# Kernel optimization log

Hardware: AMD Instinct MI355X
Metric: run time of the kernel (lower is better)

Reference implementation:

```python
import jax, jax.numpy as jnp
import numpy as np

N, E, D = 50000, 600000, 128
LN_EPS = 1e-5


def setup_inputs() -> dict:
    key = jax.random.key(0)
    ks = jax.random.split(key, 7)
    s = 1.0 / np.sqrt(D)
    x = jax.random.normal(ks[0], (N, D), dtype=jnp.float32)
    edge_index = jax.random.randint(ks[1], (2, E), 0, N, dtype=jnp.int32)
    Wq = jax.random.normal(ks[2], (D, D), dtype=jnp.float32) * s
    Wk = jax.random.normal(ks[3], (D, D), dtype=jnp.float32) * s
    Wv = jax.random.normal(ks[4], (D, D), dtype=jnp.float32) * s
    Wo = jax.random.normal(ks[5], (D, D), dtype=jnp.float32) * s
    bo = jnp.zeros((D,), dtype=jnp.float32)
    gamma = jnp.ones((D,), dtype=jnp.float32)
    beta = jnp.zeros((D,), dtype=jnp.float32)
    return {"x": x, "edge_index": edge_index, "Wq": Wq, "Wk": Wk,
            "Wv": Wv, "Wo": Wo, "bo": bo, "gamma": gamma, "beta": beta}


def reference(x, edge_index, Wq, Wk, Wv, Wo, bo, gamma, beta):
    src, dst = edge_index[0], edge_index[1]
    # gather endpoint features, project (torch Linear: y = x @ W.T)
    q = x[dst] @ Wq.T                      # [E, D]
    k = x[src] @ Wk.T                      # [E, D]
    v = x[src] @ Wv.T                      # [E, D]
    logits = jnp.sum(q * k, axis=-1, keepdims=True) / np.sqrt(D)  # [E, 1]
    msg = jax.nn.sigmoid(logits) * v       # [E, D]
    agg = jax.ops.segment_sum(msg, dst, num_segments=N)  # scatter-add -> [N, D]
    out = agg @ Wo.T + bo
    h = x + out
    # LayerNorm over last dim
    mu = jnp.mean(h, axis=-1, keepdims=True)
    var = jnp.mean(jnp.square(h - mu), axis=-1, keepdims=True)
    return (h - mu) * jax.lax.rsqrt(var + LN_EPS) * gamma + beta
```

## Files before the change

### kernel.cpp

```cpp
#include <hip/hip_runtime.h>
#include <math.h>


#define BM 64
#define NB 8

typedef __attribute__((ext_vector_type(8))) short bfrag;
typedef __attribute__((ext_vector_type(4))) float f32x4;

__device__ __forceinline__ short f2bf(float f) {
    union { float f; unsigned u; } v; v.f = f;
    unsigned r = v.u + 0x7FFFu + ((v.u >> 16) & 1u);
    return (short)(r >> 16);
}
__device__ __forceinline__ float bf2f(short h) {
    union { unsigned u; float f; } v;
    v.u = ((unsigned)(unsigned short)h) << 16;
    return v.f;
}
__device__ __forceinline__ float2 bfpair(unsigned w) {
    union { unsigned u; float f; } lo, hi;
    lo.u = w << 16;
    hi.u = w & 0xffff0000u;
    return make_float2(lo.f, hi.f);
}

__global__ __launch_bounds__(256) void zero_prep(
    const float* __restrict__ Wq, const float* __restrict__ Wk,
    const float* __restrict__ Wv, const float* __restrict__ Wo,
    short* __restrict__ whi, short* __restrict__ wlo,
    int* __restrict__ hist, int N)
{
    int g = blockIdx.x * 256 + threadIdx.x;
    if (g < N) hist[g] = 0;
    if (g < 65536) {
        const float* Ws[4] = {Wq, Wk, Wv, Wo};
        float f = Ws[g >> 14][g & 16383];
        short h = f2bf(f);
        short l = f2bf(f - bf2f(h));
        whi[g] = h; wlo[g] = l;
    }
}

__global__ __launch_bounds__(256) void qkv_mfma(
    const float* __restrict__ x,
    const short* __restrict__ whi, const short* __restrict__ wlo,
    float* __restrict__ Q, unsigned short* __restrict__ KV16, int N)
{
    __shared__ short xs_hi[64][136];
    __shared__ short xs_lo[64][136];

    const int tid = threadIdx.x;
    const int row0 = blockIdx.x * BM;

    #pragma unroll
    for (int i = 0; i < 8; ++i) {
        int idx = tid + 256 * i;
        int r = idx >> 5;
        int c4 = idx & 31;
        int gr = row0 + r;
        float4 val = make_float4(0.f, 0.f, 0.f, 0.f);
        if (gr < N) val = ((const float4*)(x + (size_t)gr * 128))[c4];
        short4 h, l;
        h.x = f2bf(val.x); l.x = f2bf(val.x - bf2f(h.x));
        h.y = f2bf(val.y); l.y = f2bf(val.y - bf2f(h.y));
        h.z = f2bf(val.z); l.z = f2bf(val.z - bf2f(h.z));
        h.w = f2bf(val.w); l.w = f2bf(val.w - bf2f(h.w));
        *((short4*)&xs_hi[r][c4 * 4]) = h;
        *((short4*)&xs_lo[r][c4 * 4]) = l;
    }
    __syncthreads();

    const int wid  = tid >> 6;
    const int lane = tid & 63;
    const int n16  = lane & 15;
    const int quad = lane >> 4;

    #pragma unroll 1
    for (int mat = 0; mat < 3; ++mat) {
        const short* __restrict__ WH = whi + mat * 16384;
        const short* __restrict__ WL = wlo + mat * 16384;
        const f32x4 zero = {0.f, 0.f, 0.f, 0.f};
        f32x4 acc[4][2];
        #pragma unroll
        for (int t = 0; t < 4; ++t) { acc[t][0] = zero; acc[t][1] = zero; }

        #pragma unroll
        for (int kc = 0; kc < 4; ++kc) {
            int k0 = kc * 32 + quad * 8;
            bfrag ah[4], al[4], bh[2], bl[2];
            #pragma unroll
            for (int t = 0; t < 4; ++t) {
                ah[t] = *((const bfrag*)&xs_hi[t * 16 + n16][k0]);
                al[t] = *((const bfrag*)&xs_lo[t * 16 + n16][k0]);
            }
            #pragma unroll
            for (int c = 0; c < 2; ++c) {
                int wr = (wid * 2 + c) * 16 + n16;
                bh[c] = *((const bfrag*)(WH + wr * 128 + k0));
                bl[c] = *((const bfrag*)(WL + wr * 128 + k0));
            }
            #pragma unroll
            for (int t = 0; t < 4; ++t)
                #pragma unroll
                for (int c = 0; c < 2; ++c) {
                    acc[t][c] = __builtin_amdgcn_mfma_f32_16x16x32_bf16(ah[t], bh[c], acc[t][c], 0, 0, 0);
                    acc[t][c] = __builtin_amdgcn_mfma_f32_16x16x32_bf16(al[t], bh[c], acc[t][c], 0, 0, 0);
                    acc[t][c] = __builtin_amdgcn_mfma_f32_16x16x32_bf16(ah[t], bl[c], acc[t][c], 0, 0, 0);
                }
        }
        #pragma unroll
        for (int t = 0; t < 4; ++t)
            #pragma unroll
            for (int r = 0; r < 4; ++r) {
                int grow = row0 + t * 16 + quad * 4 + r;
                if (grow < N) {
                    int c0 = (wid * 2 + 0) * 16 + n16;
                    int c1 = (wid * 2 + 1) * 16 + n16;
                    if (mat == 0) {
                        Q[(size_t)grow * 128 + c0] = acc[t][0][r];
                        Q[(size_t)grow * 128 + c1] = acc[t][1][r];
                    } else {
                        size_t base = (size_t)grow * 256 + (mat - 1);
                        KV16[base + 2 * c0] = (unsigned short)f2bf(acc[t][0][r]);
                        KV16[base + 2 * c1] = (unsigned short)f2bf(acc[t][1][r]);
                    }
                }
            }
    }
}

__global__ __launch_bounds__(256) void hist_kernel(
    const int* __restrict__ ei, int* __restrict__ hist, int E)
{
    int e = blockIdx.x * blockDim.x + threadIdx.x;
    if (e < E) atomicAdd(&hist[ei[E + e]], 1);
}

#define SCAN_TPB 256
#define SCAN_EPT 4

__global__ __launch_bounds__(SCAN_TPB) void scan_partial(
    const int* __restrict__ hist, int* __restrict__ offs,
    int* __restrict__ blockSums, int N)
{
    __shared__ int sdata[SCAN_TPB];
    int b = blockIdx.x;
    int t = threadIdx.x;
    int base = b * SCAN_TPB * SCAN_EPT + t * SCAN_EPT;
    int v[SCAN_EPT];
    int tot = 0;
    #pragma unroll
    for (int j = 0; j < SCAN_EPT; ++j) {
        int idx = base + j;
        v[j] = (idx < N) ? hist[idx] : 0;
        tot += v[j];
    }
    sdata[t] = tot;
    __syncthreads();
    for (int off = 1; off < SCAN_TPB; off <<= 1) {
        int xv = (t >= off) ? sdata[t - off] : 0;
        __syncthreads();
        sdata[t] += xv;
        __syncthreads();
    }
    int run = sdata[t] - tot;
    #pragma unroll
    for (int j = 0; j < SCAN_EPT; ++j) {
        int idx = base + j;
        if (idx < N) offs[idx] = run;
        run += v[j];
    }
    if (t == SCAN_TPB - 1) blockSums[b] = sdata[t];
}

__global__ __launch_bounds__(256) void scan_blocksums(int* __restrict__ blockSums, int nb)
{
    __shared__ int sdata[256];
    int t = threadIdx.x;
    int orig = (t < nb) ? blockSums[t] : 0;
    sdata[t] = orig;
    __syncthreads();
    for (int off = 1; off < 256; off <<= 1) {
        int xv = (t >= off) ? sdata[t - off] : 0;
        __syncthreads();
        sdata[t] += xv;
        __syncthreads();
    }
    if (t < nb) blockSums[t] = sdata[t] - orig;
}

__global__ __launch_bounds__(256) void scan_add(
    int* __restrict__ offs, int* __restrict__ starts,
    const int* __restrict__ blockSums, int N)
{
    int idx = blockIdx.x * blockDim.x + threadIdx.x;
    if (idx < N) {
        int vv = offs[idx] + blockSums[idx >> 10];
        offs[idx] = vv;
        starts[idx] = vv;
    }
}

__global__ __launch_bounds__(256) void scatter_kernel(
    const int* __restrict__ ei, int* __restrict__ offs,
    int* __restrict__ ssrc, int E)
{
    int e = blockIdx.x * blockDim.x + threadIdx.x;
    if (e < E) {
        int d = ei[E + e];
        int pos = atomicAdd(&offs[d], 1);
        ssrc[pos] = ei[e];
    }
}

__global__ __launch_bounds__(256) void node_agg(
    const int* __restrict__ ssrc,
    const int* __restrict__ starts,
    const int* __restrict__ endoffs,
    const float* __restrict__ Q, const unsigned short* __restrict__ KV16,
    float* __restrict__ agg, int N)
{
    int node = blockIdx.x * 4 + (threadIdx.x >> 6);
    int lane = threadIdx.x & 63;
    if (node >= N) return;
    int start = starts[node];
    int end = endoffs[node];
    float2 q = *((const float2*)(Q + (size_t)node * 128 + lane * 2));
    float a0 = 0.f, a1 = 0.f;

    for (int i = start; i < end; i += NB) {
        int s[NB];
        #pragma unroll
        for (int j = 0; j < NB; ++j) {
            int idx = i + j;
            idx = (idx < end) ? idx : (end - 1);
            s[j] = ssrc[idx];
        }
        uint2 w[NB];
        #pragma unroll
        for (int j = 0; j < NB; ++j)
            w[j] = *((const uint2*)(KV16 + (size_t)s[j] * 256 + lane * 4));
        float p[NB];
        #pragma unroll
        for (int j = 0; j < NB; ++j) {
            float2 kv0 = bfpair(w[j].x);
            float2 kv1 = bfpair(w[j].y);
            p[j] = q.x * kv0.x + q.y * kv1.x;
        }
        #pragma unroll
        for (int j = 0; j < NB; ++j)
            p[j] += __int_as_float(__builtin_amdgcn_ds_swizzle(__float_as_int(p[j]), 0x041F));
        #pragma unroll
        for (int j = 0; j < NB; ++j)
            p[j] += __int_as_float(__builtin_amdgcn_ds_swizzle(__float_as_int(p[j]), 0x081F));
        #pragma unroll
        for (int j = 0; j < NB; ++j)
            p[j] += __int_as_float(__builtin_amdgcn_ds_swizzle(__float_as_int(p[j]), 0x101F));
        #pragma unroll
        for (int j = 0; j < NB; ++j)
            p[j] += __int_as_float(__builtin_amdgcn_ds_swizzle(__float_as_int(p[j]), 0x201F));
        #pragma unroll
        for (int j = 0; j < NB; ++j)
            p[j] += __int_as_float(__builtin_amdgcn_ds_swizzle(__float_as_int(p[j]), 0x401F));
        #pragma unroll
        for (int j = 0; j < NB; ++j)
            p[j] += __shfl_xor(p[j], 32);

        #pragma unroll
        for (int j = 0; j < NB; ++j) {
            float c = 1.f / (1.f + __expf(-p[j] * 0.0883883476483184f));
            if (i + j >= end) c = 0.f;
            float2 kv0 = bfpair(w[j].x);
            float2 kv1 = bfpair(w[j].y);
            a0 += c * kv0.y; a1 += c * kv1.y;
        }
    }
    *((float2*)(agg + (size_t)node * 128 + lane * 2)) = make_float2(a0, a1);
}

__global__ __launch_bounds__(256) void out_ln_mfma(
    const float* __restrict__ agg,
    const short* __restrict__ whi, const short* __restrict__ wlo,
    const float* __restrict__ bo, const float* __restrict__ x,
    const float* __restrict__ gamma, const float* __restrict__ beta,
    float* __restrict__ out, int N)
{
    __shared__ __align__(16) char smem[64 * 136 * 2 * 2];
    short (*xs_hi)[136] = (short(*)[136])smem;
    short (*xs_lo)[136] = (short(*)[136])(smem + 64 * 136 * 2);
    float (*hs)[132]    = (float(*)[132])smem;

    const int tid = threadIdx.x;
    const int row0 = blockIdx.x * BM;

    #pragma unroll
    for (int i = 0; i < 8; ++i) {
        int idx = tid + 256 * i;
        int r = idx >> 5;
        int c4 = idx & 31;
        int gr = row0 + r;
        float4 val = make_float4(0.f, 0.f, 0.f, 0.f);
        if (gr < N) val = ((const float4*)(agg + (size_t)gr * 128))[c4];
        short4 h, l;
        h.x = f2bf(val.x); l.x = f2bf(val.x - bf2f(h.x));
        h.y = f2bf(val.y); l.y = f2bf(val.y - bf2f(h.y));
        h.z = f2bf(val.z); l.z = f2bf(val.z - bf2f(h.z));
        h.w = f2bf(val.w); l.w = f2bf(val.w - bf2f(h.w));
        *((short4*)&xs_hi[r][c4 * 4]) = h;
        *((short4*)&xs_lo[r][c4 * 4]) = l;
    }
    __syncthreads();

    const int wid  = tid >> 6;
    const int lane = tid & 63;
    const int n16  = lane & 15;
    const int quad = lane >> 4;
    const short* __restrict__ WH = whi + 3 * 16384;
    const short* __restrict__ WL = wlo + 3 * 16384;

    const f32x4 zero = {0.f, 0.f, 0.f, 0.f};
    f32x4 acc[4][2];
    #pragma unroll
    for (int t = 0; t < 4; ++t) { acc[t][0] = zero; acc[t][1] = zero; }

    #pragma unroll
    for (int kc = 0; kc < 4; ++kc) {
        int k0 = kc * 32 + quad * 8;
        bfrag ah[4], al[4], bh[2], bl[2];
        #pragma unroll
        for (int t = 0; t < 4; ++t) {
            ah[t] = *((const bfrag*)&xs_hi[t * 16 + n16][k0]);
            al[t] = *((const bfrag*)&xs_lo[t * 16 + n16][k0]);
        }
        #pragma unroll
        for (int c = 0; c < 2; ++c) {
            int wr = (wid * 2 + c) * 16 + n16;
            bh[c] = *((const bfrag*)(WH + wr * 128 + k0));
            bl[c] = *((const bfrag*)(WL + wr * 128 + k0));
        }
        #pragma unroll
        for (int t = 0; t < 4; ++t)
            #pragma unroll
            for (int c = 0; c < 2; ++c) {
                acc[t][c] = __builtin_amdgcn_mfma_f32_16x16x32_bf16(ah[t], bh[c], acc[t][c], 0, 0, 0);
                acc[t][c] = __builtin_amdgcn_mfma_f32_16x16x32_bf16(al[t], bh[c], acc[t][c], 0, 0, 0);
                acc[t][c] = __builtin_amdgcn_mfma_f32_16x16x32_bf16(ah[t], bl[c], acc[t][c], 0, 0, 0);
            }
    }
    __syncthreads();

    #pragma unroll
    for (int t = 0; t < 4; ++t)
        #pragma unroll
        for (int r = 0; r < 4; ++r) {
            hs[t * 16 + quad * 4 + r][(wid * 2 + 0) * 16 + n16] = acc[t][0][r];
            hs[t * 16 + quad * 4 + r][(wid * 2 + 1) * 16 + n16] = acc[t][1][r];
        }
    __syncthreads();

    {
        int r = tid >> 2;
        int qd = tid & 3;
        int gr = row0 + r;
        float sum = 0.f, sq = 0.f;
        #pragma unroll
        for (int c = 0; c < 32; c += 4) {
            float4 g4 = *((float4*)&hs[r][qd * 32 + c]);
            float4 b4 = *((const float4*)(bo + qd * 32 + c));
            float4 x4 = make_float4(0.f, 0.f, 0.f, 0.f);
            if (gr < N) x4 = *((const float4*)(x + (size_t)gr * 128 + qd * 32 + c));
            float4 h = make_float4(g4.x + b4.x + x4.x, g4.y + b4.y + x4.y,
                                   g4.z + b4.z + x4.z, g4.w + b4.w + x4.w);
            *((float4*)&hs[r][qd * 32 + c]) = h;
            sum += h.x + h.y + h.z + h.w;
            sq += h.x * h.x + h.y * h.y + h.z * h.z + h.w * h.w;
        }
        sum += __shfl_xor(sum, 1); sum += __shfl_xor(sum, 2);
        sq  += __shfl_xor(sq, 1);  sq  += __shfl_xor(sq, 2);
        float mu = sum * (1.f / 128.f);
        float var = sq * (1.f / 128.f) - mu * mu;
        float rs = rsqrtf(var + 1e-5f);
        if (gr < N) {
            #pragma unroll
            for (int c = 0; c < 32; c += 4) {
                float4 h = *((float4*)&hs[r][qd * 32 + c]);
                float4 g = *((const float4*)(gamma + qd * 32 + c));
                float4 b = *((const float4*)(beta + qd * 32 + c));
                float4 o = make_float4((h.x - mu) * rs * g.x + b.x,
                                       (h.y - mu) * rs * g.y + b.y,
                                       (h.z - mu) * rs * g.z + b.z,
                                       (h.w - mu) * rs * g.w + b.w);
                *((float4*)(out + (size_t)gr * 128 + qd * 32 + c)) = o;
            }
        }
    }
}

extern "C" void kernel_launch(void* const* d_in, const int* in_sizes, int n_in,
                              void* d_out, int out_size, void* d_ws, size_t ws_size,
                              hipStream_t stream) {
    const float* x     = (const float*)d_in[0];
    const int*   ei    = (const int*)d_in[1];
    const float* Wq    = (const float*)d_in[2];
    const float* Wk    = (const float*)d_in[3];
    const float* Wv    = (const float*)d_in[4];
    const float* Wo    = (const float*)d_in[5];
    const float* bo    = (const float*)d_in[6];
    const float* gamma = (const float*)d_in[7];
    const float* beta  = (const float*)d_in[8];
    const int N = in_sizes[0] / 128;
    const int E = in_sizes[1] / 2;
    const size_t ND = (size_t)N * 128;

    float* ws  = (float*)d_ws;
    float* Q   = ws;
    unsigned short* KV16 = (unsigned short*)(Q + ND);
    float* agg = (float*)(KV16 + 2 * ND);
    int* hist      = (int*)(agg + ND);
    int* offs      = hist + N;
    int* starts    = offs + N;
    int* blockSums = starts + N;
    int* ssrc      = blockSums + 256;
    short* whi     = (short*)(ssrc + E);
    short* wlo     = whi + 4 * 16384;

    const int gzp = ((N > 65536 ? N : 65536) + 255) / 256;
    zero_prep<<<gzp, 256, 0, stream>>>(Wq, Wk, Wv, Wo, whi, wlo, hist, N);

    hist_kernel<<<(E + 255) / 256, 256, 0, stream>>>(ei, hist, E);
    const int nScanBlocks = (N + SCAN_TPB * SCAN_EPT - 1) / (SCAN_TPB * SCAN_EPT);
    scan_partial<<<nScanBlocks, SCAN_TPB, 0, stream>>>(hist, offs, blockSums, N);
    scan_blocksums<<<1, 256, 0, stream>>>(blockSums, nScanBlocks);
    scan_add<<<(N + 255) / 256, 256, 0, stream>>>(offs, starts, blockSums, N);
    scatter_kernel<<<(E + 255) / 256, 256, 0, stream>>>(ei, offs, ssrc, E);

    const int gq = (N + BM - 1) / BM;
    qkv_mfma<<<gq, 256, 0, stream>>>(x, whi, wlo, Q, KV16, N);

    node_agg<<<(N + 3) / 4, 256, 0, stream>>>(ssrc, starts, offs, Q, KV16, agg, N);

    out_ln_mfma<<<gq, 256, 0, stream>>>(agg, whi, wlo, bo, x, gamma, beta,
                                        (float*)d_out, N);
}
```

Measured before the change: 281.5 us.

## Split wavefront into 4 edge groups of 16 lanes in node aggregation

The node aggregation kernel now has each wavefront process 4 edges at a time, twice per iteration, with 16 lanes per edge. Each lane loads 32 bytes of interleaved K/V and reduces over 16 lanes instead of 64, so there are fewer swizzle steps per edge. Partial accumulators from the four edge groups are combined once at the end. The Q projection now stores Q pre-multiplied by the negated 1/sqrt(D) factor, and the sigmoid uses a fast reciprocal. This cuts cross-lane reduction work and raises memory parallelism per edge, at the cost of more registers and an extra reduction at the end.

Result: no change. 280.8 us (-0.2%).

```diff
diff --git a/kernel.cpp b/kernel.cpp
--- a/kernel.cpp
+++ b/kernel.cpp
@@ -3,7 +3,7 @@
 
 
 #define BM 64
-#define NB 8
+#define QSCALE -0.08838834764831845f
 
 typedef __attribute__((ext_vector_type(8))) short bfrag;
 typedef __attribute__((ext_vector_type(4))) float f32x4;
@@ -18,12 +18,14 @@
     v.u = ((unsigned)(unsigned short)h) << 16;
     return v.f;
 }
-__device__ __forceinline__ float2 bfpair(unsigned w) {
-    union { unsigned u; float f; } lo, hi;
-    lo.u = w << 16;
-    hi.u = w & 0xffff0000u;
-    return make_float2(lo.f, hi.f);
-}
+__device__ __forceinline__ float klo(unsigned w) {
+    union { unsigned u; float f; } v; v.u = w << 16; return v.f;
+}
+__device__ __forceinline__ float vhi(unsigned w) {
+    union { unsigned u; float f; } v; v.u = w & 0xffff0000u; return v.f;
+}
+
+#define SWZ(x, pat) __int_as_float(__builtin_amdgcn_ds_swizzle(__float_as_int(x), pat))
 
 __global__ __launch_bounds__(256) void zero_prep(
     const float* __restrict__ Wq, const float* __restrict__ Wk,
@@ -118,8 +120,8 @@
                     int c0 = (wid * 2 + 0) * 16 + n16;
                     int c1 = (wid * 2 + 1) * 16 + n16;
                     if (mat == 0) {
-                        Q[(size_t)grow * 128 + c0] = acc[t][0][r];
-                        Q[(size_t)grow * 128 + c1] = acc[t][1][r];
+                        Q[(size_t)grow * 128 + c0] = acc[t][0][r] * QSCALE;
+                        Q[(size_t)grow * 128 + c1] = acc[t][1][r] * QSCALE;
                     } else {
                         size_t base = (size_t)grow * 256 + (mat - 1);
                         KV16[base + 2 * c0] = (unsigned short)f2bf(acc[t][0][r]);
@@ -222,61 +224,88 @@
     float* __restrict__ agg, int N)
 {
     int node = blockIdx.x * 4 + (threadIdx.x >> 6);
+    if (node >= N) return;
     int lane = threadIdx.x & 63;
-    if (node >= N) return;
+    int eg   = lane >> 4;
+    int sl   = lane & 15;
     int start = starts[node];
-    int end = endoffs[node];
-    float2 q = *((const float2*)(Q + (size_t)node * 128 + lane * 2));
-    float a0 = 0.f, a1 = 0.f;
-
-    for (int i = start; i < end; i += NB) {
-        int s[NB];
-        #pragma unroll
-        for (int j = 0; j < NB; ++j) {
-            int idx = i + j;
-            idx = (idx < end) ? idx : (end - 1);
-            s[j] = ssrc[idx];
-        }
-        uint2 w[NB];
-        #pragma unroll
-        for (int j = 0; j < NB; ++j)
-            w[j] = *((const uint2*)(KV16 + (size_t)s[j] * 256 + lane * 4));
-        float p[NB];
-        #pragma unroll
-        for (int j = 0; j < NB; ++j) {
-            float2 kv0 = bfpair(w[j].x);
-            float2 kv1 = bfpair(w[j].y);
-            p[j] = q.x * kv0.x + q.y * kv1.x;
-        }
-        #pragma unroll
-        for (int j = 0; j < NB; ++j)
-            p[j] += __int_as_float(__builtin_amdgcn_ds_swizzle(__float_as_int(p[j]), 0x041F));
-        #pragma unroll
-        for (int j = 0; j < NB; ++j)
-            p[j] += __int_as_float(__builtin_amdgcn_ds_swizzle(__float_as_int(p[j]), 0x081F));
-        #pragma unroll
-        for (int j = 0; j < NB; ++j)
-            p[j] += __int_as_float(__builtin_amdgcn_ds_swizzle(__float_as_int(p[j]), 0x101F));
-        #pragma unroll
-        for (int j = 0; j < NB; ++j)
-            p[j] += __int_as_float(__builtin_amdgcn_ds_swizzle(__float_as_int(p[j]), 0x201F));
-        #pragma unroll
-        for (int j = 0; j < NB; ++j)
-            p[j] += __int_as_float(__builtin_amdgcn_ds_swizzle(__float_as_int(p[j]), 0x401F));
-        #pragma unroll
-        for (int j = 0; j < NB; ++j)
-            p[j] += __shfl_xor(p[j], 32);
-
-        #pragma unroll
-        for (int j = 0; j < NB; ++j) {
-            float c = 1.f / (1.f + __expf(-p[j] * 0.0883883476483184f));
-            if (i + j >= end) c = 0.f;
-            float2 kv0 = bfpair(w[j].x);
-            float2 kv1 = bfpair(w[j].y);
-            a0 += c * kv0.y; a1 += c * kv1.y;
-        }
-    }
-    *((float2*)(agg + (size_t)node * 128 + lane * 2)) = make_float2(a0, a1);
+    int end   = endoffs[node];
+
+    const float4 q0 = *((const float4*)(Q + (size_t)node * 128 + sl * 8));
+    const float4 q1 = *((const float4*)(Q + (size_t)node * 128 + sl * 8 + 4));
+
+    float a0 = 0.f, a1 = 0.f, a2 = 0.f, a3 = 0.f;
+    float a4 = 0.f, a5 = 0.f, a6 = 0.f, a7 = 0.f;
+
+    const unsigned short* kvbase = KV16 + sl * 16;
+
+    for (int i = start; i < end; i += 8) {
+        int i0 = i + eg;
+        int i1 = i + 4 + eg;
+        int ok0 = (i0 < end);
+        int ok1 = (i1 < end);
+        i0 = ok0 ? i0 : (end - 1);
+        i1 = ok1 ? i1 : (end - 1);
+        int s0 = ssrc[i0];
+        int s1 = ssrc[i1];
+        const unsigned short* kp0 = kvbase + ((size_t)s0 << 8);
+        const unsigned short* kp1 = kvbase + ((size_t)s1 << 8);
+        uint4 wa0 = *((const uint4*)kp0);
+        uint4 wa1 = *((const uint4*)(kp0 + 8));
+        uint4 wb0 = *((const uint4*)kp1);
+        uint4 wb1 = *((const uint4*)(kp1 + 8));
+
+        float p0, p1;
+        p0 = q0.x * klo(wa0.x);
+        p0 = fmaf(q0.y, klo(wa0.y), p0);
+        p0 = fmaf(q0.z, klo(wa0.z), p0);
+        p0 = fmaf(q0.w, klo(wa0.w), p0);
+        p0 = fmaf(q1.x, klo(wa1.x), p0);
+        p0 = fmaf(q1.y, klo(wa1.y), p0);
+        p0 = fmaf(q1.z, klo(wa1.z), p0);
+        p0 = fmaf(q1.w, klo(wa1.w), p0);
+        p1 = q0.x * klo(wb0.x);
+        p1 = fmaf(q0.y, klo(wb0.y), p1);
+        p1 = fmaf(q0.z, klo(wb0.z), p1);
+        p1 = fmaf(q0.w, klo(wb0.w), p1);
+        p1 = fmaf(q1.x, klo(wb1.x), p1);
+        p1 = fmaf(q1.y, klo(wb1.y), p1);
+        p1 = fmaf(q1.z, klo(wb1.z), p1);
+        p1 = fmaf(q1.w, klo(wb1.w), p1);
+
+        p0 += SWZ(p0, 0x041F); p1 += SWZ(p1, 0x041F);
+        p0 += SWZ(p0, 0x081F); p1 += SWZ(p1, 0x081F);
+        p0 += SWZ(p0, 0x101F); p1 += SWZ(p1, 0x101F);
+        p0 += SWZ(p0, 0x201F); p1 += SWZ(p1, 0x201F);
+
+        float c0 = __builtin_amdgcn_rcpf(1.f + __expf(p0));
+        float c1 = __builtin_amdgcn_rcpf(1.f + __expf(p1));
+        if (!ok0) c0 = 0.f;
+        if (!ok1) c1 = 0.f;
+
+        a0 = fmaf(c0, vhi(wa0.x), a0); a0 = fmaf(c1, vhi(wb0.x), a0);
+        a1 = fmaf(c0, vhi(wa0.y), a1); a1 = fmaf(c1, vhi(wb0.y), a1);
+        a2 = fmaf(c0, vhi(wa0.z), a2); a2 = fmaf(c1, vhi(wb0.z), a2);
+        a3 = fmaf(c0, vhi(wa0.w), a3); a3 = fmaf(c1, vhi(wb0.w), a3);
+        a4 = fmaf(c0, vhi(wa1.x), a4); a4 = fmaf(c1, vhi(wb1.x), a4);
+        a5 = fmaf(c0, vhi(wa1.y), a5); a5 = fmaf(c1, vhi(wb1.y), a5);
+        a6 = fmaf(c0, vhi(wa1.z), a6); a6 = fmaf(c1, vhi(wb1.z), a6);
+        a7 = fmaf(c0, vhi(wa1.w), a7); a7 = fmaf(c1, vhi(wb1.w), a7);
+    }
+
+    a0 += SWZ(a0, 0x401F); a1 += SWZ(a1, 0x401F);
+    a2 += SWZ(a2, 0x401F); a3 += SWZ(a3, 0x401F);
+    a4 += SWZ(a4, 0x401F); a5 += SWZ(a5, 0x401F);
+    a6 += SWZ(a6, 0x401F); a7 += SWZ(a7, 0x401F);
+    a0 += __shfl_xor(a0, 32); a1 += __shfl_xor(a1, 32);
+    a2 += __shfl_xor(a2, 32); a3 += __shfl_xor(a3, 32);
+    a4 += __shfl_xor(a4, 32); a5 += __shfl_xor(a5, 32);
+    a6 += __shfl_xor(a6, 32); a7 += __shfl_xor(a7, 32);
+
+    if (eg == 0) {
+        *((float4*)(agg + (size_t)node * 128 + sl * 8))     = make_float4(a0, a1, a2, a3);
+        *((float4*)(agg + (size_t)node * 128 + sl * 8 + 4)) = make_float4(a4, a5, a6, a7);
+    }
 }
 
 __global__ __launch_bounds__(256) void out_ln_mfma(
```
